# Kernel tuning notes

Measured on AMD Instinct MI355X. Metric: run time of the kernel, lower is better.

The kernel has to match this reference:

```python
import jax, jax.numpy as jnp
import numpy as np

NHEADS = 8
HEAD_DIM = 64  # odim // nheads = 512 // 8


def setup_inputs() -> dict:
    key = jax.random.key(0)
    ks = jax.random.split(key, 5)
    B, S, D = 2, 4096, 512
    scale = 1.0 / np.sqrt(D)
    return {
        "m_feats": jax.random.normal(ks[0], (B, S, D), dtype=jnp.float32),
        "Wc": jax.random.normal(ks[1], (2 * D, D), dtype=jnp.float32) * scale,
        "bc": jax.random.normal(ks[2], (2 * D,), dtype=jnp.float32) * 0.01,
        "Wv": jax.random.normal(ks[3], (D, D), dtype=jnp.float32) * scale,
        "bv": jax.random.normal(ks[4], (D,), dtype=jnp.float32) * 0.01,
    }


def reference(m_feats, Wc, bc, Wv, bv):
    # eval mode: dropout(p=0.5) is identity
    B, S, D = m_feats.shape
    H, Dh = NHEADS, HEAD_DIM
    m_k = m_feats @ Wv.T + bv                    # [B,S,D]
    m_trans = m_feats @ Wc.T + bc                # [B,S,2D]
    m_q, m_v = m_trans[..., :D], m_trans[..., D:]
    # torch.split into contiguous per-head chunks == reshape to [B,S,H,Dh]
    k = m_k.reshape(B, S, H, Dh)
    q = m_q.reshape(B, S, H, Dh)
    v = m_v.reshape(B, S, H, Dh)
    # scores[b,h,i,j] = k_i . q_j / sqrt(Dh); softmax over j (the q axis)
    scores = jnp.einsum("bihd,bjhd->bhij", k, q) / np.sqrt(Dh).astype(np.float32)
    w = jax.nn.softmax(scores, axis=-1)          # [B,H,S,S]
    r = jnp.einsum("bhij,bjhd->bihd", w, v).reshape(B, S, D)
    return m_feats + r
```

## Files before the change

kernel.cpp:

```cpp
#include <hip/hip_runtime.h>

#define MTOT 8192

typedef __attribute__((ext_vector_type(8))) short bf16x8;
typedef __attribute__((ext_vector_type(4))) float f32x4;

#if __has_builtin(__builtin_amdgcn_exp2f)
#define EXP2F __builtin_amdgcn_exp2f
#else
#define EXP2F exp2f
#endif

#define SC 0.18033688011112042f
#define LDP 72

static __device__ __forceinline__ unsigned short f2b(float f) {
  union { float f; unsigned int i; } x;
  x.f = f;
  unsigned int i = x.i;
  return (unsigned short)((i + 0x7FFFu + ((i >> 16) & 1u)) >> 16);
}
static __device__ __forceinline__ unsigned int pkt(float a, float b) {
  union { float f; unsigned int i; } xa, xb;
  xa.f = a; xb.f = b;
  return (xa.i >> 16) | (xb.i & 0xFFFF0000u);
}
static __device__ __forceinline__ bf16x8 ld8f32_bf16(const float* __restrict__ p) {
  f32x4 lo = *(const f32x4*)p;
  f32x4 hi = *(const f32x4*)(p + 4);
  union { unsigned int u[4]; bf16x8 v; } r;
  r.u[0] = pkt(lo[0], lo[1]);
  r.u[1] = pkt(lo[2], lo[3]);
  r.u[2] = pkt(hi[0], hi[1]);
  r.u[3] = pkt(hi[2], hi[3]);
  return r.v;
}

__global__ __launch_bounds__(256) void gemm_qv(
    const float* __restrict__ mf,
    const float* __restrict__ Wc,
    const float* __restrict__ bc,
    unsigned short* __restrict__ qvws)
{
  const int bid = blockIdx.x;
  const int tn = bid & 7, tm = bid >> 3;
  const int w = threadIdx.x >> 6, lane = threadIdx.x & 63;
  const int n = lane & 15, q = lane >> 4;
  const int row0 = tm * 128 + (w >> 1) * 64;
  const int col0 = tn * 128 + (w & 1) * 64;

  f32x4 acc[4][4] = {};

  for (int kk = 0; kk < 512; kk += 32) {
    bf16x8 a[4], b[4];
#pragma unroll
    for (int si = 0; si < 4; ++si)
      a[si] = ld8f32_bf16(mf + (size_t)(row0 + si * 16 + n) * 512 + kk + q * 8);
#pragma unroll
    for (int sj = 0; sj < 4; ++sj) {
      const int nb = col0 + sj * 16 + n;
      b[sj] = ld8f32_bf16(Wc + (size_t)nb * 512 + kk + q * 8);
    }
#pragma unroll
    for (int si = 0; si < 4; ++si)
#pragma unroll
      for (int sj = 0; sj < 4; ++sj)
        acc[si][sj] = __builtin_amdgcn_mfma_f32_16x16x32_bf16(a[si], b[sj], acc[si][sj], 0, 0, 0);
  }

#pragma unroll
  for (int sj = 0; sj < 4; ++sj) {
    const int nb = col0 + sj * 16 + n;
    const float bias = bc[nb];
    const int sector = nb >> 9;
    const int d = nb & 511;
    const int h = d >> 6, dh = d & 63;
    unsigned short* dst = qvws + (size_t)sector * MTOT * 512;
#pragma unroll
    for (int si = 0; si < 4; ++si) {
#pragma unroll
      for (int r = 0; r < 4; ++r) {
        const int srow = row0 + si * 16 + q * 4 + r;
        const int b_ = srow >> 12, s_ = srow & 4095;
        dst[(size_t)((b_ * 8 + h) * 4096 + s_) * 64 + dh] = f2b(acc[si][sj][r] + bias);
      }
    }
  }
}

__global__ __launch_bounds__(256) void attn_kernel(
    const unsigned short* __restrict__ qvws,
    const float* __restrict__ mf,
    const float* __restrict__ Wv,
    const float* __restrict__ bv,
    float* __restrict__ out)
{
  const unsigned short* Qw = qvws;
  const unsigned short* Vw = qvws + (size_t)MTOT * 512;

  const int bid = blockIdx.x;
  const int bh = bid >> 5;
  const int ib = bid & 31;
  const int b_ = bh >> 3, h = bh & 7;
  const int w = threadIdx.x >> 6, lane = threadIdx.x & 63;
  const int n = lane & 15, q = lane >> 4;
  const int i0w = ib * 128 + w * 32;

  __shared__ alignas(16) unsigned short Qs[64 * LDP];
  __shared__ alignas(16) unsigned short Vt[64 * LDP];
  __shared__ alignas(16) unsigned short PK[4][32 * LDP];

  {
    f32x4 ka[2][4] = {};
    for (int kk = 0; kk < 512; kk += 32) {
      bf16x8 a0 = ld8f32_bf16(mf + (size_t)(b_ * 4096 + i0w + n) * 512 + kk + q * 8);
      bf16x8 a1 = ld8f32_bf16(mf + (size_t)(b_ * 4096 + i0w + 16 + n) * 512 + kk + q * 8);
#pragma unroll
      for (int t = 0; t < 4; ++t) {
        bf16x8 bw = ld8f32_bf16(Wv + (size_t)(h * 64 + t * 16 + n) * 512 + kk + q * 8);
        ka[0][t] = __builtin_amdgcn_mfma_f32_16x16x32_bf16(a0, bw, ka[0][t], 0, 0, 0);
        ka[1][t] = __builtin_amdgcn_mfma_f32_16x16x32_bf16(a1, bw, ka[1][t], 0, 0, 0);
      }
    }
#pragma unroll
    for (int sub = 0; sub < 2; ++sub)
#pragma unroll
      for (int t = 0; t < 4; ++t) {
        const float bias = bv[h * 64 + t * 16 + n];
#pragma unroll
        for (int r = 0; r < 4; ++r)
          PK[w][(sub * 16 + q * 4 + r) * LDP + t * 16 + n] = f2b((ka[sub][t][r] + bias) * SC);
      }
  }
  __syncthreads();

  bf16x8 aK[2][2];
#pragma unroll
  for (int sub = 0; sub < 2; ++sub)
#pragma unroll
    for (int s = 0; s < 2; ++s)
      aK[sub][s] = *(const bf16x8*)(&PK[w][(sub * 16 + n) * LDP + s * 32 + q * 8]);

  f32x4 o[2][4] = {};
  f32x4 lacc[2] = {};
  const bf16x8 ones = {(short)0x3F80, (short)0x3F80, (short)0x3F80, (short)0x3F80,
                       (short)0x3F80, (short)0x3F80, (short)0x3F80, (short)0x3F80};

  const int qjr = threadIdx.x >> 2;
  const int qc = (threadIdx.x & 3) * 8;
  const int vjp = threadIdx.x & 31;
  const int vdq = (threadIdx.x >> 5) * 8;

  const unsigned short* Qsrc = Qw + (size_t)(bh * 4096 + qjr) * 64 + qc;
  const unsigned short* Vsrc = Vw + (size_t)(bh * 4096 + 2 * vjp) * 64 + vdq;

  bf16x8 pq0 = *(const bf16x8*)(Qsrc);
  bf16x8 pq1 = *(const bf16x8*)(Qsrc + 32);
  bf16x8 pv0 = *(const bf16x8*)(Vsrc);
  bf16x8 pv1 = *(const bf16x8*)(Vsrc + 64);

  for (int j0 = 0; j0 < 4096; j0 += 64) {
    __syncthreads();
    *(bf16x8*)(&Qs[qjr * LDP + qc]) = pq0;
    *(bf16x8*)(&Qs[qjr * LDP + qc + 32]) = pq1;
#pragma unroll
    for (int e = 0; e < 8; ++e) {
      unsigned int pk = (unsigned int)(unsigned short)pv0[e] |
                        ((unsigned int)(unsigned short)pv1[e] << 16);
      *(unsigned int*)(&Vt[(vdq + e) * LDP + 2 * vjp]) = pk;
    }
    __syncthreads();

    {
      const size_t jn = (size_t)((j0 + 64) & 4095) * 64;
      pq0 = *(const bf16x8*)(Qsrc + jn);
      pq1 = *(const bf16x8*)(Qsrc + jn + 32);
      pv0 = *(const bf16x8*)(Vsrc + jn);
      pv1 = *(const bf16x8*)(Vsrc + jn + 64);
    }

    bf16x8 bq[4][2], bvv[4][2];
#pragma unroll
    for (int jt = 0; jt < 4; ++jt)
#pragma unroll
      for (int s = 0; s < 2; ++s)
        bq[jt][s] = *(const bf16x8*)(&Qs[(jt * 16 + n) * LDP + s * 32 + q * 8]);
#pragma unroll
    for (int t = 0; t < 4; ++t)
#pragma unroll
      for (int s = 0; s < 2; ++s)
        bvv[t][s] = *(const bf16x8*)(&Vt[(t * 16 + n) * LDP + s * 32 + q * 8]);

    f32x4 c[2][4] = {};
#pragma unroll
    for (int sub = 0; sub < 2; ++sub)
#pragma unroll
      for (int jt = 0; jt < 4; ++jt)
#pragma unroll
        for (int s = 0; s < 2; ++s)
          c[sub][jt] = __builtin_amdgcn_mfma_f32_16x16x32_bf16(bq[jt][s], aK[sub][s], c[sub][jt], 0, 0, 0);

#pragma unroll
    for (int sub = 0; sub < 2; ++sub)
#pragma unroll
      for (int jt = 0; jt < 4; ++jt) {
        uint2 pk;
        pk.x = pkt(EXP2F(c[sub][jt][0]), EXP2F(c[sub][jt][1]));
        pk.y = pkt(EXP2F(c[sub][jt][2]), EXP2F(c[sub][jt][3]));
        *(uint2*)(&PK[w][(sub * 16 + n) * LDP + jt * 16 + q * 4]) = pk;
      }
    asm volatile("s_waitcnt lgkmcnt(0)" ::: "memory");

#pragma unroll
    for (int sub = 0; sub < 2; ++sub) {
      bf16x8 pa0 = *(const bf16x8*)(&PK[w][(sub * 16 + n) * LDP + q * 8]);
      bf16x8 pa1 = *(const bf16x8*)(&PK[w][(sub * 16 + n) * LDP + 32 + q * 8]);
      lacc[sub] = __builtin_amdgcn_mfma_f32_16x16x32_bf16(pa0, ones, lacc[sub], 0, 0, 0);
      lacc[sub] = __builtin_amdgcn_mfma_f32_16x16x32_bf16(pa1, ones, lacc[sub], 0, 0, 0);
#pragma unroll
      for (int t = 0; t < 4; ++t) {
        o[sub][t] = __builtin_amdgcn_mfma_f32_16x16x32_bf16(pa0, bvv[t][0], o[sub][t], 0, 0, 0);
        o[sub][t] = __builtin_amdgcn_mfma_f32_16x16x32_bf16(pa1, bvv[t][1], o[sub][t], 0, 0, 0);
      }
    }
  }

#pragma unroll
  for (int sub = 0; sub < 2; ++sub) {
    f32x4 linv;
#pragma unroll
    for (int r = 0; r < 4; ++r) linv[r] = 1.0f / lacc[sub][r];
#pragma unroll
    for (int t = 0; t < 4; ++t) {
#pragma unroll
      for (int r = 0; r < 4; ++r) {
        const int i = i0w + sub * 16 + q * 4 + r;
        const int dh = t * 16 + n;
        const size_t idx = (size_t)(b_ * 4096 + i) * 512 + h * 64 + dh;
        out[idx] = o[sub][t][r] * linv[r] + mf[idx];
      }
    }
  }
}

extern "C" void kernel_launch(void* const* d_in, const int* in_sizes, int n_in,
                              void* d_out, int out_size, void* d_ws, size_t ws_size,
                              hipStream_t stream) {
  const float* mf = (const float*)d_in[0];
  const float* Wc = (const float*)d_in[1];
  const float* bc = (const float*)d_in[2];
  const float* Wv = (const float*)d_in[3];
  const float* bv = (const float*)d_in[4];
  float* out = (float*)d_out;
  unsigned short* qvws = (unsigned short*)d_ws;

  gemm_qv<<<512, 256, 0, stream>>>(mf, Wc, bc, qvws);
  attn_kernel<<<512, 256, 0, stream>>>(qvws, mf, Wv, bv, out);
}
```

Measured before the change: 275.1 us.

## Split attention keys across waves, read Q/V from global, pre-transpose V

```diff
diff --git a/kernel.cpp b/kernel.cpp
--- a/kernel.cpp
+++ b/kernel.cpp
@@ -13,6 +13,7 @@
 
 #define SC 0.18033688011112042f
 #define LDP 72
+#define CTS 136
 
 static __device__ __forceinline__ unsigned short f2b(float f) {
   union { float f; unsigned int i; } x;
@@ -68,53 +69,90 @@
         acc[si][sj] = __builtin_amdgcn_mfma_f32_16x16x32_bf16(a[si], b[sj], acc[si][sj], 0, 0, 0);
   }
 
-#pragma unroll
-  for (int sj = 0; sj < 4; ++sj) {
-    const int nb = col0 + sj * 16 + n;
-    const float bias = bc[nb];
-    const int sector = nb >> 9;
-    const int d = nb & 511;
-    const int h = d >> 6, dh = d & 63;
-    unsigned short* dst = qvws + (size_t)sector * MTOT * 512;
-#pragma unroll
-    for (int si = 0; si < 4; ++si) {
-#pragma unroll
-      for (int r = 0; r < 4; ++r) {
-        const int srow = row0 + si * 16 + q * 4 + r;
-        const int b_ = srow >> 12, s_ = srow & 4095;
-        dst[(size_t)((b_ * 8 + h) * 4096 + s_) * 64 + dh] = f2b(acc[si][sj][r] + bias);
-      }
-    }
-  }
-}
-
-__global__ __launch_bounds__(256) void attn_kernel(
+  __shared__ alignas(16) unsigned short Ct[128 * CTS];
+  const bool isV = (tn >= 4);
+  const int rl0 = (w >> 1) * 64;
+  const int cl0 = (w & 1) * 64;
+
+  if (!isV) {
+#pragma unroll
+    for (int sj = 0; sj < 4; ++sj) {
+      const float bias = bc[col0 + sj * 16 + n];
+#pragma unroll
+      for (int si = 0; si < 4; ++si)
+#pragma unroll
+        for (int r = 0; r < 4; ++r)
+          Ct[(rl0 + si * 16 + q * 4 + r) * CTS + cl0 + sj * 16 + n] =
+              f2b(acc[si][sj][r] + bias);
+    }
+  } else {
+#pragma unroll
+    for (int sj = 0; sj < 4; ++sj) {
+      const float bias = bc[col0 + sj * 16 + n];
+#pragma unroll
+      for (int si = 0; si < 4; ++si) {
+        uint2 pk;
+        pk.x = pkt(acc[si][sj][0] + bias, acc[si][sj][1] + bias);
+        pk.y = pkt(acc[si][sj][2] + bias, acc[si][sj][3] + bias);
+        *(uint2*)(&Ct[(cl0 + sj * 16 + n) * CTS + rl0 + si * 16 + q * 4]) = pk;
+      }
+    }
+  }
+  __syncthreads();
+
+  const int rk = threadIdx.x & 7;
+  const int rr = threadIdx.x >> 3;
+#pragma unroll
+  for (int rp = 0; rp < 4; ++rp) {
+    const int row = rp * 32 + rr;
+#pragma unroll
+    for (int ch = 0; ch < 2; ++ch) {
+      const int col = ch * 64 + rk * 8;
+      bf16x8 v = *(const bf16x8*)(&Ct[row * CTS + col]);
+      if (!isV) {
+        const int srow = tm * 128 + row;
+        const int bb = srow >> 12, ss = srow & 4095;
+        const int nbg = tn * 128 + col;
+        const int hh = nbg >> 6, dh0 = nbg & 63;
+        *(bf16x8*)(qvws + ((size_t)((bb * 8 + hh) * 4096 + ss)) * 64 + dh0) = v;
+      } else {
+        const int nbv = tn * 128 + row - 512;
+        const int hh = nbv >> 6, dh0 = nbv & 63;
+        const int scol = tm * 128 + col;
+        const int bb = scol >> 12, ss = scol & 4095;
+        *(bf16x8*)(qvws + (size_t)MTOT * 512 +
+                   ((size_t)((bb * 8 + hh) * 64 + dh0)) * 4096 + ss) = v;
+      }
+    }
+  }
+}
+
+__global__ __launch_bounds__(128, 2) void attn_kernel(
     const unsigned short* __restrict__ qvws,
     const float* __restrict__ mf,
     const float* __restrict__ Wv,
     const float* __restrict__ bv,
     float* __restrict__ out)
 {
-  const unsigned short* Qw = qvws;
-  const unsigned short* Vw = qvws + (size_t)MTOT * 512;
-
   const int bid = blockIdx.x;
-  const int bh = bid >> 5;
-  const int ib = bid & 31;
+  const int bh = bid >> 6;
+  const int ib = bid & 63;
   const int b_ = bh >> 3, h = bh & 7;
   const int w = threadIdx.x >> 6, lane = threadIdx.x & 63;
   const int n = lane & 15, q = lane >> 4;
-  const int i0w = ib * 128 + w * 32;
-
-  __shared__ alignas(16) unsigned short Qs[64 * LDP];
-  __shared__ alignas(16) unsigned short Vt[64 * LDP];
-  __shared__ alignas(16) unsigned short PK[4][32 * LDP];
+  const int i0 = ib * 64;
+
+  __shared__ alignas(16) unsigned short PK[2][64 * LDP];
+  __shared__ float lbuf[64];
+
+  const unsigned short* Qb = qvws + (size_t)(bh * 4096) * 64;
+  const unsigned short* Vb = qvws + (size_t)MTOT * 512 + (size_t)(bh * 64) * 4096;
 
   {
     f32x4 ka[2][4] = {};
     for (int kk = 0; kk < 512; kk += 32) {
-      bf16x8 a0 = ld8f32_bf16(mf + (size_t)(b_ * 4096 + i0w + n) * 512 + kk + q * 8);
-      bf16x8 a1 = ld8f32_bf16(mf + (size_t)(b_ * 4096 + i0w + 16 + n) * 512 + kk + q * 8);
+      bf16x8 a0 = ld8f32_bf16(mf + (size_t)(b_ * 4096 + i0 + (2 * w + 0) * 16 + n) * 512 + kk + q * 8);
+      bf16x8 a1 = ld8f32_bf16(mf + (size_t)(b_ * 4096 + i0 + (2 * w + 1) * 16 + n) * 512 + kk + q * 8);
 #pragma unroll
       for (int t = 0; t < 4; ++t) {
         bf16x8 bw = ld8f32_bf16(Wv + (size_t)(h * 64 + t * 16 + n) * 512 + kk + q * 8);
@@ -123,121 +161,110 @@
       }
     }
 #pragma unroll
-    for (int sub = 0; sub < 2; ++sub)
+    for (int sl = 0; sl < 2; ++sl)
 #pragma unroll
       for (int t = 0; t < 4; ++t) {
         const float bias = bv[h * 64 + t * 16 + n];
 #pragma unroll
         for (int r = 0; r < 4; ++r)
-          PK[w][(sub * 16 + q * 4 + r) * LDP + t * 16 + n] = f2b((ka[sub][t][r] + bias) * SC);
-      }
-  }
-  __syncthreads();
-
-  bf16x8 aK[2][2];
-#pragma unroll
-  for (int sub = 0; sub < 2; ++sub)
+          PK[0][((2 * w + sl) * 16 + q * 4 + r) * LDP + t * 16 + n] =
+              f2b((ka[sl][t][r] + bias) * SC);
+      }
+  }
+  __syncthreads();
+  bf16x8 aK[4][2];
+#pragma unroll
+  for (int sub = 0; sub < 4; ++sub)
 #pragma unroll
     for (int s = 0; s < 2; ++s)
-      aK[sub][s] = *(const bf16x8*)(&PK[w][(sub * 16 + n) * LDP + s * 32 + q * 8]);
-
-  f32x4 o[2][4] = {};
-  f32x4 lacc[2] = {};
+      aK[sub][s] = *(const bf16x8*)(&PK[0][(sub * 16 + n) * LDP + s * 32 + q * 8]);
+  __syncthreads();
+
+  f32x4 o[4][4] = {};
+  f32x4 lacc[4] = {};
   const bf16x8 ones = {(short)0x3F80, (short)0x3F80, (short)0x3F80, (short)0x3F80,
                        (short)0x3F80, (short)0x3F80, (short)0x3F80, (short)0x3F80};
-
-  const int qjr = threadIdx.x >> 2;
-  const int qc = (threadIdx.x & 3) * 8;
-  const int vjp = threadIdx.x & 31;
-  const int vdq = (threadIdx.x >> 5) * 8;
-
-  const unsigned short* Qsrc = Qw + (size_t)(bh * 4096 + qjr) * 64 + qc;
-  const unsigned short* Vsrc = Vw + (size_t)(bh * 4096 + 2 * vjp) * 64 + vdq;
-
-  bf16x8 pq0 = *(const bf16x8*)(Qsrc);
-  bf16x8 pq1 = *(const bf16x8*)(Qsrc + 32);
-  bf16x8 pv0 = *(const bf16x8*)(Vsrc);
-  bf16x8 pv1 = *(const bf16x8*)(Vsrc + 64);
-
-  for (int j0 = 0; j0 < 4096; j0 += 64) {
-    __syncthreads();
-    *(bf16x8*)(&Qs[qjr * LDP + qc]) = pq0;
-    *(bf16x8*)(&Qs[qjr * LDP + qc + 32]) = pq1;
-#pragma unroll
-    for (int e = 0; e < 8; ++e) {
-      unsigned int pk = (unsigned int)(unsigned short)pv0[e] |
-                        ((unsigned int)(unsigned short)pv1[e] << 16);
-      *(unsigned int*)(&Vt[(vdq + e) * LDP + 2 * vjp]) = pk;
-    }
-    __syncthreads();
-
-    {
-      const size_t jn = (size_t)((j0 + 64) & 4095) * 64;
-      pq0 = *(const bf16x8*)(Qsrc + jn);
-      pq1 = *(const bf16x8*)(Qsrc + jn + 32);
-      pv0 = *(const bf16x8*)(Vsrc + jn);
-      pv1 = *(const bf16x8*)(Vsrc + jn + 64);
-    }
-
-    bf16x8 bq[4][2], bvv[4][2];
+  unsigned short* Pw = &PK[w][0];
+
+  for (int it = 0; it < 32; ++it) {
+    const int j0 = w * 2048 + it * 64;
+
+    bf16x8 bq[4][2];
 #pragma unroll
     for (int jt = 0; jt < 4; ++jt)
 #pragma unroll
       for (int s = 0; s < 2; ++s)
-        bq[jt][s] = *(const bf16x8*)(&Qs[(jt * 16 + n) * LDP + s * 32 + q * 8]);
-#pragma unroll
-    for (int t = 0; t < 4; ++t)
-#pragma unroll
-      for (int s = 0; s < 2; ++s)
-        bvv[t][s] = *(const bf16x8*)(&Vt[(t * 16 + n) * LDP + s * 32 + q * 8]);
-
-    f32x4 c[2][4] = {};
-#pragma unroll
-    for (int sub = 0; sub < 2; ++sub)
+        bq[jt][s] = *(const bf16x8*)(Qb + (size_t)(j0 + jt * 16 + n) * 64 + s * 32 + q * 8);
+
+#pragma unroll
+    for (int sub = 0; sub < 4; ++sub) {
+      f32x4 c[4] = {};
 #pragma unroll
       for (int jt = 0; jt < 4; ++jt)
 #pragma unroll
         for (int s = 0; s < 2; ++s)
-          c[sub][jt] = __builtin_amdgcn_mfma_f32_16x16x32_bf16(bq[jt][s], aK[sub][s], c[sub][jt], 0, 0, 0);
-
-#pragma unroll
-    for (int sub = 0; sub < 2; ++sub)
+          c[jt] = __builtin_amdgcn_mfma_f32_16x16x32_bf16(bq[jt][s], aK[sub][s], c[jt], 0, 0, 0);
 #pragma unroll
       for (int jt = 0; jt < 4; ++jt) {
         uint2 pk;
-        pk.x = pkt(EXP2F(c[sub][jt][0]), EXP2F(c[sub][jt][1]));
-        pk.y = pkt(EXP2F(c[sub][jt][2]), EXP2F(c[sub][jt][3]));
-        *(uint2*)(&PK[w][(sub * 16 + n) * LDP + jt * 16 + q * 4]) = pk;
-      }
+        pk.x = pkt(EXP2F(c[jt][0]), EXP2F(c[jt][1]));
+        pk.y = pkt(EXP2F(c[jt][2]), EXP2F(c[jt][3]));
+        *(uint2*)(Pw + (sub * 16 + n) * LDP + jt * 16 + q * 4) = pk;
+      }
+    }
     asm volatile("s_waitcnt lgkmcnt(0)" ::: "memory");
 
 #pragma unroll
-    for (int sub = 0; sub < 2; ++sub) {
-      bf16x8 pa0 = *(const bf16x8*)(&PK[w][(sub * 16 + n) * LDP + q * 8]);
-      bf16x8 pa1 = *(const bf16x8*)(&PK[w][(sub * 16 + n) * LDP + 32 + q * 8]);
-      lacc[sub] = __builtin_amdgcn_mfma_f32_16x16x32_bf16(pa0, ones, lacc[sub], 0, 0, 0);
-      lacc[sub] = __builtin_amdgcn_mfma_f32_16x16x32_bf16(pa1, ones, lacc[sub], 0, 0, 0);
+    for (int s = 0; s < 2; ++s) {
+      bf16x8 bvv[4];
+#pragma unroll
+      for (int t = 0; t < 4; ++t)
+        bvv[t] = *(const bf16x8*)(Vb + (size_t)(t * 16 + n) * 4096 + j0 + s * 32 + q * 8);
+#pragma unroll
+      for (int sub = 0; sub < 4; ++sub) {
+        bf16x8 pa = *(const bf16x8*)(Pw + (sub * 16 + n) * LDP + s * 32 + q * 8);
+        lacc[sub] = __builtin_amdgcn_mfma_f32_16x16x32_bf16(pa, ones, lacc[sub], 0, 0, 0);
+#pragma unroll
+        for (int t = 0; t < 4; ++t)
+          o[sub][t] = __builtin_amdgcn_mfma_f32_16x16x32_bf16(pa, bvv[t], o[sub][t], 0, 0, 0);
+      }
+    }
+  }
+
+  __syncthreads();
+  float* mO = (float*)&PK[0][0];
+  if (w == 1) {
+#pragma unroll
+    for (int sub = 0; sub < 4; ++sub) {
+#pragma unroll
+      for (int t = 0; t < 4; ++t)
+#pragma unroll
+        for (int r = 0; r < 4; ++r)
+          mO[(sub * 16 + q * 4 + r) * 68 + t * 16 + n] = o[sub][t][r];
+      if (n == 0)
+#pragma unroll
+        for (int r = 0; r < 4; ++r)
+          lbuf[sub * 16 + q * 4 + r] = lacc[sub][r];
+    }
+  }
+  __syncthreads();
+  if (w == 0) {
+#pragma unroll
+    for (int sub = 0; sub < 4; ++sub) {
+      float li[4];
+#pragma unroll
+      for (int r = 0; r < 4; ++r)
+        li[r] = 1.0f / (lacc[sub][r] + lbuf[sub * 16 + q * 4 + r]);
 #pragma unroll
       for (int t = 0; t < 4; ++t) {
-        o[sub][t] = __builtin_amdgcn_mfma_f32_16x16x32_bf16(pa0, bvv[t][0], o[sub][t], 0, 0, 0);
-        o[sub][t] = __builtin_amdgcn_mfma_f32_16x16x32_bf16(pa1, bvv[t][1], o[sub][t], 0, 0, 0);
-      }
-    }
-  }
-
-#pragma unroll
-  for (int sub = 0; sub < 2; ++sub) {
-    f32x4 linv;
-#pragma unroll
-    for (int r = 0; r < 4; ++r) linv[r] = 1.0f / lacc[sub][r];
-#pragma unroll
-    for (int t = 0; t < 4; ++t) {
-#pragma unroll
-      for (int r = 0; r < 4; ++r) {
-        const int i = i0w + sub * 16 + q * 4 + r;
-        const int dh = t * 16 + n;
-        const size_t idx = (size_t)(b_ * 4096 + i) * 512 + h * 64 + dh;
-        out[idx] = o[sub][t][r] * linv[r] + mf[idx];
+#pragma unroll
+        for (int r = 0; r < 4; ++r) {
+          const int i = i0 + sub * 16 + q * 4 + r;
+          const int dh = t * 16 + n;
+          const size_t idx = (size_t)(b_ * 4096 + i) * 512 + h * 64 + dh;
+          out[idx] = (o[sub][t][r] + mO[(sub * 16 + q * 4 + r) * 68 + t * 16 + n]) * li[r]
+                     + mf[idx];
+        }
       }
     }
   }
@@ -255,5 +282,5 @@
   unsigned short* qvws = (unsigned short*)d_ws;
 
   gemm_qv<<<512, 256, 0, stream>>>(mf, Wc, bc, qvws);
-  attn_kernel<<<512, 256, 0, stream>>>(qvws, mf, Wv, bv, out);
-}
+  attn_kernel<<<1024, 128, 0, stream>>>(qvws, mf, Wv, bv, out);
+}
```

After: 292.6 us. 1.06x slower.
